# Performance work log

Measured on AMD Instinct MI355X. Metric: run time of the kernel, lower is better.

The kernel has to match this reference:

```python
import jax, jax.numpy as jnp
import numpy as np

TEMP = 0.1   # temperature
EPS = 1e-5   # BatchNorm eps
NEG = -1e9   # mask value for excluded logits

def _conv3x3(x, w):
    return jax.lax.conv_general_dilated(x, w, (1, 1), 'SAME',
                                        dimension_numbers=('NCHW', 'OIHW', 'NCHW'))

def _bn(x, gamma, beta, axes):
    # training-mode BatchNorm2d: stats over `axes` (per-sample (2,3) for the
    # single-sample anchor path, batch (0,2,3) for the dense-key path)
    m = x.mean(axes, keepdims=True)
    v = x.var(axes, keepdims=True)
    return gamma[None, :, None, None] * (x - m) * jax.lax.rsqrt(v + EPS) + beta[None, :, None, None]

def _encode(x, p, axes):
    # GranularityEncoder: conv3x3 -> BN -> ReLU -> conv1x1 -> BN -> ReLU -> GAP
    w1, g1, b1, w2, g2, b2 = p
    h = jax.nn.relu(_bn(_conv3x3(x, w1), g1, b1, axes))
    h = jnp.einsum('nchw,oc->nohw', h, w2)
    h = jax.nn.relu(_bn(h, g2, b2, axes))
    return h.mean((2, 3))  # [N, D]

def _norm(x):
    return x / jnp.maximum(jnp.linalg.norm(x, axis=-1, keepdims=True), 1e-12)

def _loss(sparse, dense, params, decision_mask):
    # Anchors: original encodes one sample at a time -> per-sample BN stats (2,3)
    Q = jnp.stack([_norm(_encode(s, p, (2, 3))) for s, p in zip(sparse, params)])        # [G,cav,D]
    # Dense keys: encoded as a full batch under no_grad -> batch BN stats, stop_gradient
    K = jax.lax.stop_gradient(
        jnp.stack([_norm(_encode(d, p, (0, 2, 3))) for d, p in zip(dense, params)]))     # [G,cav,D]
    S = jnp.einsum('gid,gjd->gij', Q, K)                     # same-granularity sims
    pos = jnp.diagonal(S, axis1=1, axis2=2)                  # [G,cav] l_pos
    cav = S.shape[1]
    S_m = jnp.where(jnp.eye(cav, dtype=bool)[None], NEG, S)  # inter-agent negatives (j != i)
    X = jnp.einsum('gid,hid->gih', Q, K)                     # cross-granularity, same agent
    X_m = jnp.where(jnp.eye(3, dtype=bool)[:, None, :], NEG, X)
    logits = jnp.concatenate([pos[..., None], S_m, X_m], axis=-1) / TEMP  # [G,cav,1+cav+3]
    loss_tab = -logits[..., 0] + jax.nn.logsumexp(logits, axis=-1)        # CE with label 0
    # The per-element loss only depends on (agent, granularity): weight by mask counts.
    cnt = jnp.stack([(decision_mask == g + 1).sum((1, 2)) for g in range(3)]).astype(jnp.float32)  # [G,cav-1]
    cnt = jnp.pad(cnt, ((0, 0), (1, 0)))  # agent 0 is never an anchor (loop starts at i=1)
    tot = cnt.sum()
    return jnp.where(tot > 0, (cnt * loss_tab).sum() / jnp.maximum(tot, 1.0), 0.0)

def setup_inputs():
    key = jax.random.key(0)
    ks = jax.random.split(key, 16)
    CAV, H, W, D = 5, 256, 256, 128
    C = {'g1': 64, 'g2': 32, 'g3': 16}
    inp = {}
    i = 0
    for name, c in C.items():
        inp['sparse_' + name] = jax.random.normal(ks[i], (CAV, c, H, W), jnp.float32); i += 1
        inp['dense_' + name] = jax.random.normal(ks[i], (CAV, c, H, W), jnp.float32); i += 1
        inp['w1_' + name] = jax.random.normal(ks[i], (64, c, 3, 3), jnp.float32) * 0.05; i += 1
        inp['bn1_gamma_' + name] = jnp.ones((64,), jnp.float32)
        inp['bn1_beta_' + name] = jnp.zeros((64,), jnp.float32)
        inp['w2_' + name] = jax.random.normal(ks[i], (D, 64), jnp.float32) * 0.05; i += 1
        inp['bn2_gamma_' + name] = jnp.ones((D,), jnp.float32)
        inp['bn2_beta_' + name] = jnp.zeros((D,), jnp.float32)
    inp['decision_mask'] = jax.random.randint(ks[i], (CAV - 1, 128, 128), 0, 4, jnp.int32)
    return inp

def reference(sparse_g1, dense_g1, w1_g1, bn1_gamma_g1, bn1_beta_g1, w2_g1, bn2_gamma_g1, bn2_beta_g1,
              sparse_g2, dense_g2, w1_g2, bn1_gamma_g2, bn1_beta_g2, w2_g2, bn2_gamma_g2, bn2_beta_g2,
              sparse_g3, dense_g3, w1_g3, bn1_gamma_g3, bn1_beta_g3, w2_g3, bn2_gamma_g3, bn2_beta_g3,
              decision_mask):
    sparse = [sparse_g1, sparse_g2, sparse_g3]
    dense = [dense_g1, dense_g2, dense_g3]
    params = [(w1_g1, bn1_gamma_g1, bn1_beta_g1, w2_g1, bn2_gamma_g1, bn2_beta_g1),
              (w1_g2, bn1_gamma_g2, bn1_beta_g2, w2_g2, bn2_gamma_g2, bn2_beta_g2),
              (w1_g3, bn1_gamma_g3, bn1_beta_g3, w2_g3, bn2_gamma_g3, bn2_beta_g3)]
    return _loss(sparse, dense, params, decision_mask)
```

## Files before the change

### kernel.cpp

```cpp
#include <hip/hip_runtime.h>
#include <math.h>

#define HW 65536
#define NS 5
#define DFEAT 128
#define CMID 64
#define TEMPER 0.1f
#define BNEPS 1e-5f

#define SWZ(a) ((a) ^ ((((a) >> 7) & 7) << 4))

typedef __attribute__((ext_vector_type(8))) short bf16x8;
typedef __attribute__((ext_vector_type(4))) float f32x4;

__device__ inline short f2bf(float f) {
  union { float f; unsigned u; } v; v.f = f;
  unsigned r = v.u + 0x7fffu + ((v.u >> 16) & 1u);
  return (short)(r >> 16);
}
__device__ inline float bf2f(unsigned short h) {
  union { unsigned u; float f; } v; v.u = ((unsigned)h) << 16;
  return v.f;
}

union U16B { int4 v; unsigned short s[8]; };

__global__ void zero_kernel(float* __restrict__ p, int n) {
  int i = blockIdx.x * blockDim.x + threadIdx.x;
  if (i < n) p[i] = 0.f;
}

template<int C, int CP>
__global__ __launch_bounds__(256) void transpose_kernel(const float* __restrict__ x,
                                                        unsigned short* __restrict__ xT,
                                                        float* __restrict__ st) {
  __shared__ float t[64 * (CP + 1)];
  const int tid = threadIdx.x;
  if (blockIdx.x == 0 && blockIdx.y == 0) {
    for (int i = tid; i < 1920; i += 256) st[i] = 0.f;
  }
  const int n = blockIdx.y;
  const int pix0 = blockIdx.x * 64;
  const float* xn = x + (size_t)n * C * HW + pix0;
#pragma unroll
  for (int it = 0; it < CP * 64 / 256; ++it) {
    int idx = it * 256 + tid;
    int c = idx >> 6, pix = idx & 63;
    float v = (c < C) ? xn[(size_t)c * HW + pix] : 0.f;
    t[pix * (CP + 1) + c] = v;
  }
  __syncthreads();
  unsigned* out = (unsigned*)(xT + ((size_t)n * HW + pix0) * CP);
#pragma unroll
  for (int it = 0; it < 64 * CP / 2 / 256; ++it) {
    int idx = it * 256 + tid;
    int cp = idx & (CP / 2 - 1), pix = idx / (CP / 2);
    float f0 = t[pix * (CP + 1) + 2 * cp];
    float f1 = t[pix * (CP + 1) + 2 * cp + 1];
    unsigned u = ((unsigned)(unsigned short)f2bf(f0)) |
                 (((unsigned)(unsigned short)f2bf(f1)) << 16);
    out[pix * (CP / 2) + cp] = u;
  }
}

template<int C, int CP>
__global__ void wprep_kernel(const float* __restrict__ w1, const float* __restrict__ w2,
                             unsigned short* __restrict__ w1p, unsigned short* __restrict__ w2p) {
  const int KS = CP / 32;
  const int total1 = 9 * KS * 2 * 64 * 32;
  int idx = blockIdx.x * 256 + threadIdx.x;
  if (idx < total1) {
    int kl = idx & 31; int tmp = idx >> 5;
    int nn = tmp & 63; tmp >>= 6;
    int hl = tmp & 1;  tmp >>= 1;
    int ks = tmp % KS; int s = tmp / KS;
    int ic = ks * 32 + kl;
    float v = (ic < C) ? w1[((size_t)nn * C + ic) * 9 + s] : 0.f;
    short hi = f2bf(v);
    short r = (hl == 0) ? hi : f2bf(v - bf2f((unsigned short)hi));
    w1p[idx] = (unsigned short)r;
  } else if (idx < total1 + 2 * 2 * 128 * 32) {
    int i2 = idx - total1;
    int kl = i2 & 31;
    int nn = (i2 >> 5) & 127;
    int hl = (i2 >> 12) & 1;
    int ks = i2 >> 13;
    float v = w2[nn * 64 + ks * 32 + kl];
    short hi = f2bf(v);
    short r = (hl == 0) ? hi : f2bf(v - bf2f((unsigned short)hi));
    w2p[i2] = (unsigned short)r;
  }
}

template<int CP>
__global__ __launch_bounds__(256, 2) void conv_mfma_kernel(
    const unsigned short* __restrict__ xT,
    const unsigned short* __restrict__ w1p,
    unsigned short* __restrict__ h1,
    float* __restrict__ st)
{
  const int KS = CP / 32;
  constexpr int XSB = 10 * 34 * CP * 2;
  constexpr int HSB = 256 * 64 * 2;
  constexpr int UNI = (XSB > HSB) ? XSB : HSB;
  __shared__ __align__(16) char smem[UNI];
  __shared__ float reds[4][64], redq[4][64];

  const int tid = threadIdx.x;
  const int lane = tid & 63, wave = tid >> 6;
  const int lanen = lane & 15, quad = lane >> 4;
  const int tx = blockIdx.x, ty = blockIdx.y, n = blockIdx.z;
  const int x0 = tx * 32, y0 = ty * 8;

  const int ROWB = 34 * CP * 2;
  const int xstart = (tx == 0) ? 1 : 0;
  const int xend = (tx == 7) ? 33 : 34;
  for (int r = wave; r < 10; r += 4) {
    int gy = y0 - 1 + r;
    const int rowbase = r * ROWB;
    if ((unsigned)gy >= 256u) {
      for (int ofs = lane * 16; ofs < ROWB; ofs += 1024) {
        int la = rowbase + ofs;
        *(int4*)(smem + SWZ(la)) = make_int4(0, 0, 0, 0);
      }
    } else {
      const char* g = (const char*)(xT + ((size_t)n * HW + gy * 256 + x0 - 1 + xstart) * CP);
      int nbytes = (xend - xstart) * CP * 2;
      int dst0 = rowbase + xstart * CP * 2;
      for (int ofs = lane * 16; ofs < nbytes; ofs += 1024) {
        int la = dst0 + ofs;
        *(int4*)(smem + SWZ(la)) = *(const int4*)(g + ofs);
      }
      if (xstart == 1) {
        for (int ofs = lane * 16; ofs < CP * 2; ofs += 1024) {
          int la = rowbase + ofs;
          *(int4*)(smem + SWZ(la)) = make_int4(0, 0, 0, 0);
        }
      }
      if (xend == 33) {
        for (int ofs = lane * 16; ofs < CP * 2; ofs += 1024) {
          int la = rowbase + 33 * CP * 2 + ofs;
          *(int4*)(smem + SWZ(la)) = make_int4(0, 0, 0, 0);
        }
      }
    }
  }
  __syncthreads();

  f32x4 acc[4][4];
#pragma unroll
  for (int t = 0; t < 4; ++t)
#pragma unroll
    for (int nt = 0; nt < 4; ++nt)
      acc[t][nt] = (f32x4){0.f, 0.f, 0.f, 0.f};

  int pbase[4];
#pragma unroll
  for (int t = 0; t < 4; ++t) {
    int p = wave * 64 + t * 16 + lanen;
    pbase[t] = (p >> 5) * 34 + (p & 31);
  }

#pragma unroll
  for (int s = 0; s < 9; ++s) {
    const int dy = s / 3, dx = s % 3;
#pragma unroll
    for (int ks = 0; ks < KS; ++ks) {
      bf16x8 af[4];
#pragma unroll
      for (int t = 0; t < 4; ++t) {
        int la = (pbase[t] + dy * 34 + dx) * (CP * 2) + ks * 64 + quad * 16;
        af[t] = *(const bf16x8*)(smem + SWZ(la));
      }
#pragma unroll
      for (int hl = 0; hl < 2; ++hl) {
        const unsigned short* wb = w1p + ((((s * KS + ks) * 2 + hl) * 64) + lanen) * 32 + quad * 8;
#pragma unroll
        for (int nt = 0; nt < 4; ++nt) {
          bf16x8 bf = *(const bf16x8*)(wb + nt * 16 * 32);
#pragma unroll
          for (int t = 0; t < 4; ++t)
            acc[t][nt] = __builtin_amdgcn_mfma_f32_16x16x32_bf16(af[t], bf, acc[t][nt], 0, 0, 0);
        }
      }
    }
  }

#pragma unroll
  for (int nt = 0; nt < 4; ++nt) {
    float s = 0.f, q = 0.f;
#pragma unroll
    for (int t = 0; t < 4; ++t)
#pragma unroll
      for (int r = 0; r < 4; ++r) {
        float v = acc[t][nt][r];
        s += v; q += v * v;
      }
    s += __shfl_xor(s, 16); s += __shfl_xor(s, 32);
    q += __shfl_xor(q, 16); q += __shfl_xor(q, 32);
    if (lane < 16) { reds[wave][nt * 16 + lanen] = s; redq[wave][nt * 16 + lanen] = q; }
  }
  __syncthreads();
  if (tid < 64) {
    float s = reds[0][tid] + reds[1][tid] + reds[2][tid] + reds[3][tid];
    float q = redq[0][tid] + redq[1][tid] + redq[2][tid] + redq[3][tid];
    atomicAdd(&st[(n * 64 + tid) * 2 + 0], s);
    atomicAdd(&st[(n * 64 + tid) * 2 + 1], q);
  }

#pragma unroll
  for (int t = 0; t < 4; ++t)
#pragma unroll
    for (int nt = 0; nt < 4; ++nt)
#pragma unroll
      for (int r = 0; r < 4; ++r) {
        int pix = wave * 64 + t * 16 + quad * 4 + r;
        int la = pix * 128 + (nt * 16 + lanen) * 2;
        *(unsigned short*)(smem + SWZ(la)) = (unsigned short)f2bf(acc[t][nt][r]);
      }
  __syncthreads();
#pragma unroll
  for (int it = 0; it < 8; ++it) {
    int idx = it * 256 + tid;
    int ocg = idx & 7, pix = idx >> 3;
    int py = pix >> 5, px = pix & 31;
    int la = pix * 128 + ocg * 16;
    int4 v = *(const int4*)(smem + SWZ(la));
    *(int4*)(h1 + ((size_t)n * HW + (y0 + py) * 256 + x0 + px) * 64 + ocg * 8) = v;
  }
}

__device__ inline void bn_pair(const float* __restrict__ st, const float* __restrict__ gamma,
                               const float* __restrict__ beta, int nch, int n, int ch,
                               int batchmode, float& a, float& b) {
  float s, q, cnt;
  if (batchmode) {
    s = 0.f; q = 0.f;
    for (int m = 0; m < NS; ++m) { s += st[(m * nch + ch) * 2]; q += st[(m * nch + ch) * 2 + 1]; }
    cnt = (float)NS * (float)HW;
  } else {
    s = st[(n * nch + ch) * 2]; q = st[(n * nch + ch) * 2 + 1];
    cnt = (float)HW;
  }
  float mean = s / cnt;
  float var = q / cnt - mean * mean;
  float inv = rsqrtf(var + BNEPS);
  a = gamma[ch] * inv;
  b = beta[ch] - mean * a;
}

template<bool GAP>
__global__ __launch_bounds__(256, 2) void stage2_mfma_kernel(
    const unsigned short* __restrict__ h1,
    const unsigned short* __restrict__ w2p,
    const float* __restrict__ st1, const float* __restrict__ gm1, const float* __restrict__ bt1,
    const float* __restrict__ st2, const float* __restrict__ gm2, const float* __restrict__ bt2,
    int batchmode,
    float* __restrict__ out)
{
  __shared__ __align__(16) char acts[256 * 64 * 2];
  __shared__ float red[4][128], redq[4][128];
  __shared__ float s_a1[64], s_b1[64], s_a2[128], s_b2[128];
  const int tid = threadIdx.x;
  const int lane = tid & 63, wave = tid >> 6;
  const int lanen = lane & 15, quad = lane >> 4;
  const int n = blockIdx.y;
  const int pix0 = blockIdx.x * 256;

  if (tid < 64) {
    float a, b;
    bn_pair(st1, gm1, bt1, CMID, n, tid, batchmode, a, b);
    s_a1[tid] = a; s_b1[tid] = b;
  }
  if constexpr (GAP) {
    if (tid >= 64 && tid < 192) {
      int ch = tid - 64;
      float a, b;
      bn_pair(st2, gm2, bt2, DFEAT, n, ch, batchmode, a, b);
      s_a2[ch] = a; s_b2[ch] = b;
    }
  }
  __syncthreads();

  const int cg = tid & 7;
  float a1c[8], b1c[8];
#pragma unroll
  for (int j = 0; j < 8; ++j) {
    a1c[j] = s_a1[cg * 8 + j];
    b1c[j] = s_b1[cg * 8 + j];
  }
  const unsigned short* hb = h1 + ((size_t)n * HW + pix0) * 64;
#pragma unroll
  for (int it = 0; it < 8; ++it) {
    int idx = it * 256 + tid;
    int pix = idx >> 3;
    U16B in, o;
    in.v = *(const int4*)(hb + pix * 64 + cg * 8);
#pragma unroll
    for (int j = 0; j < 8; ++j) {
      float f = bf2f(in.s[j]);
      o.s[j] = (unsigned short)f2bf(fmaxf(a1c[j] * f + b1c[j], 0.f));
    }
    int la = pix * 128 + cg * 16;
    *(int4*)(acts + SWZ(la)) = o.v;
  }
  __syncthreads();

  f32x4 acc[4][8];
#pragma unroll
  for (int mt = 0; mt < 4; ++mt)
#pragma unroll
    for (int nt = 0; nt < 8; ++nt)
      acc[mt][nt] = (f32x4){0.f, 0.f, 0.f, 0.f};

#pragma unroll
  for (int ks = 0; ks < 2; ++ks) {
    bf16x8 af[4];
#pragma unroll
    for (int mt = 0; mt < 4; ++mt) {
      int la = (wave * 64 + mt * 16 + lanen) * 128 + ks * 64 + quad * 16;
      af[mt] = *(const bf16x8*)(acts + SWZ(la));
    }
#pragma unroll
    for (int hl = 0; hl < 2; ++hl) {
      const unsigned short* wb = w2p + (((ks * 2 + hl) * 128) + lanen) * 32 + quad * 8;
#pragma unroll
      for (int nt = 0; nt < 8; ++nt) {
        bf16x8 bf = *(const bf16x8*)(wb + nt * 16 * 32);
#pragma unroll
        for (int mt = 0; mt < 4; ++mt)
          acc[mt][nt] = __builtin_amdgcn_mfma_f32_16x16x32_bf16(af[mt], bf, acc[mt][nt], 0, 0, 0);
      }
    }
  }

  if constexpr (GAP) {
#pragma unroll
    for (int nt = 0; nt < 8; ++nt) {
      int o = nt * 16 + lanen;
      float a2v = s_a2[o], b2v = s_b2[o];
      float s = 0.f;
#pragma unroll
      for (int mt = 0; mt < 4; ++mt)
#pragma unroll
        for (int r = 0; r < 4; ++r)
          s += fmaxf(a2v * acc[mt][nt][r] + b2v, 0.f);
      s += __shfl_xor(s, 16); s += __shfl_xor(s, 32);
      if (lane < 16) red[wave][o] = s;
    }
    __syncthreads();
    if (tid < 128)
      atomicAdd(&out[n * DFEAT + tid], red[0][tid] + red[1][tid] + red[2][tid] + red[3][tid]);
  } else {
#pragma unroll
    for (int nt = 0; nt < 8; ++nt) {
      int o = nt * 16 + lanen;
      float s = 0.f, q = 0.f;
#pragma unroll
      for (int mt = 0; mt < 4; ++mt)
#pragma unroll
        for (int r = 0; r < 4; ++r) {
          float v = acc[mt][nt][r];
          s += v; q += v * v;
        }
      s += __shfl_xor(s, 16); s += __shfl_xor(s, 32);
      q += __shfl_xor(q, 16); q += __shfl_xor(q, 32);
      if (lane < 16) { red[wave][o] = s; redq[wave][o] = q; }
    }
    __syncthreads();
    if (tid < 128) {
      atomicAdd(&out[(n * DFEAT + tid) * 2 + 0], red[0][tid] + red[1][tid] + red[2][tid] + red[3][tid]);
      atomicAdd(&out[(n * DFEAT + tid) * 2 + 1], redq[0][tid] + redq[1][tid] + redq[2][tid] + redq[3][tid]);
    }
  }
}

__global__ void feat_kernel(const float* __restrict__ gap, float* __restrict__ QK) {
  int b = blockIdx.x;
  int e = b / 5, n = b % 5;
  int g = e >> 1, br = e & 1;
  int d = threadIdx.x;
  float v = gap[(e * 5 + n) * DFEAT + d] * (1.0f / (float)HW);
  float q = v * v;
  for (int off = 32; off; off >>= 1) q += __shfl_down(q, off, 64);
  __shared__ float r2[2];
  if ((d & 63) == 0) r2[d >> 6] = q;
  __syncthreads();
  float nrm = sqrtf(r2[0] + r2[1]);
  float inv = 1.0f / fmaxf(nrm, 1e-12f);
  QK[((br * 3 + g) * 5 + n) * DFEAT + d] = v * inv;
}

__global__ __launch_bounds__(256) void loss_kernel(const float* __restrict__ QK,
                                                   const int* __restrict__ dm,
                                                   float* __restrict__ out)
{
  __shared__ float Qs[1920], Ks[1920];
  __shared__ float S[75], X[45], cnt[15], ltab[15];
  const int tid = threadIdx.x;
  for (int i = tid; i < 1920; i += 256) { Qs[i] = QK[i]; Ks[i] = QK[1920 + i]; }
  if (tid < 15) cnt[tid] = 0.f;
  __syncthreads();
  if (tid < 75) {
    int g = tid / 25, i = (tid / 5) % 5, j = tid % 5;
    const float* q = &Qs[(g * 5 + i) * 128];
    const float* k = &Ks[(g * 5 + j) * 128];
    float s = 0.f;
    for (int d = 0; d < 128; ++d) s += q[d] * k[d];
    S[tid] = s;
  } else if (tid < 120) {
    int u = tid - 75;
    int g = u / 15, i = (u % 15) / 3, h = u % 3;
    const float* q = &Qs[(g * 5 + i) * 128];
    const float* k = &Ks[(h * 5 + i) * 128];
    float s = 0.f;
    for (int d = 0; d < 128; ++d) s += q[d] * k[d];
    X[u] = s;
  }
  {
    int a = tid >> 6, l = tid & 63;
    int c0 = 0, c1 = 0, c2 = 0;
    const int* base = dm + a * 16384;
    for (int k = 0; k < 256; ++k) {
      int v = base[k * 64 + l];
      c0 += (v == 1); c1 += (v == 2); c2 += (v == 3);
    }
    atomicAdd(&cnt[0 * 5 + a + 1], (float)c0);
    atomicAdd(&cnt[1 * 5 + a + 1], (float)c1);
    atomicAdd(&cnt[2 * 5 + a + 1], (float)c2);
  }
  __syncthreads();
  if (tid < 15) {
    int g = tid / 5, i = tid % 5;
    const float inv_t = 1.0f / TEMPER;
    float lg[9];
    lg[0] = S[g * 25 + i * 5 + i] * inv_t;
    for (int j = 0; j < 5; ++j) lg[1 + j] = (j == i) ? (-1e9f * inv_t) : S[g * 25 + i * 5 + j] * inv_t;
    for (int h = 0; h < 3; ++h) lg[6 + h] = (h == g) ? (-1e9f * inv_t) : X[g * 15 + i * 3 + h] * inv_t;
    float m = lg[0];
    for (int k = 1; k < 9; ++k) m = fmaxf(m, lg[k]);
    float se = 0.f;
    for (int k = 0; k < 9; ++k) se += expf(lg[k] - m);
    ltab[tid] = -lg[0] + m + logf(se);
  }
  __syncthreads();
  if (tid == 0) {
    float tot = 0.f, acc = 0.f;
    for (int k = 0; k < 15; ++k) { tot += cnt[k]; acc += cnt[k] * ltab[k]; }
    out[0] = (tot > 0.f) ? acc / fmaxf(tot, 1.f) : 0.f;
  }
}

extern "C" void kernel_launch(void* const* d_in, const int* in_sizes, int n_in,
                              void* d_out, int out_size, void* d_ws, size_t ws_size,
                              hipStream_t stream) {
  (void)in_sizes; (void)n_in; (void)out_size; (void)ws_size;

  const float* sp[3]  = {(const float*)d_in[0],  (const float*)d_in[8],  (const float*)d_in[16]};
  const float* dn[3]  = {(const float*)d_in[1],  (const float*)d_in[9],  (const float*)d_in[17]};
  const float* w1[3]  = {(const float*)d_in[2],  (const float*)d_in[10], (const float*)d_in[18]};
  const float* gm1[3] = {(const float*)d_in[3],  (const float*)d_in[11], (const float*)d_in[19]};
  const float* bt1[3] = {(const float*)d_in[4],  (const float*)d_in[12], (const float*)d_in[20]};
  const float* w2[3]  = {(const float*)d_in[5],  (const float*)d_in[13], (const float*)d_in[21]};
  const float* gm2[3] = {(const float*)d_in[6],  (const float*)d_in[14], (const float*)d_in[22]};
  const float* bt2[3] = {(const float*)d_in[7],  (const float*)d_in[15], (const float*)d_in[23]};
  const int*   dm     = (const int*)d_in[24];

  float* ws_f = (float*)d_ws;
  unsigned short* h1u  = (unsigned short*)ws_f;
  unsigned short* xTu  = (unsigned short*)(ws_f + 10485760);
  unsigned short* w1pu = (unsigned short*)(ws_f + 20971520);
  unsigned short* w2pu = (unsigned short*)(ws_f + 20971520 + 36864);
  float* st1 = ws_f + 20971520 + 36864 + 8192;
  float* st2 = st1 + 640;
  float* gap = st2 + 1280;
  float* QK  = gap + 3840;

  zero_kernel<<<15, 256, 0, stream>>>(gap, 3840);

  for (int g = 0; g < 3; ++g) {
    if (g == 0)      wprep_kernel<64, 64><<<(9*2*2*64*32 + 16384 + 255)/256, 256, 0, stream>>>(w1[g], w2[g], w1pu, w2pu);
    else if (g == 1) wprep_kernel<32, 32><<<(9*1*2*64*32 + 16384 + 255)/256, 256, 0, stream>>>(w1[g], w2[g], w1pu, w2pu);
    else             wprep_kernel<16, 32><<<(9*1*2*64*32 + 16384 + 255)/256, 256, 0, stream>>>(w1[g], w2[g], w1pu, w2pu);

    for (int br = 0; br < 2; ++br) {
      const int e = g * 2 + br;
      const float* x = br ? dn[g] : sp[g];

      if (g == 0)      transpose_kernel<64, 64><<<dim3(1024, 5), 256, 0, stream>>>(x, xTu, st1);
      else if (g == 1) transpose_kernel<32, 32><<<dim3(1024, 5), 256, 0, stream>>>(x, xTu, st1);
      else             transpose_kernel<16, 32><<<dim3(1024, 5), 256, 0, stream>>>(x, xTu, st1);

      if (g == 0) conv_mfma_kernel<64><<<dim3(8, 32, 5), 256, 0, stream>>>(xTu, w1pu, h1u, st1);
      else        conv_mfma_kernel<32><<<dim3(8, 32, 5), 256, 0, stream>>>(xTu, w1pu, h1u, st1);

      stage2_mfma_kernel<false><<<dim3(256, 5), 256, 0, stream>>>(
          h1u, w2pu, st1, gm1[g], bt1[g], nullptr, nullptr, nullptr, br, st2);
      stage2_mfma_kernel<true><<<dim3(256, 5), 256, 0, stream>>>(
          h1u, w2pu, st1, gm1[g], bt1[g], st2, gm2[g], bt2[g], br, gap + e * 640);
    }
  }

  feat_kernel<<<30, 128, 0, stream>>>(gap, QK);
  loss_kernel<<<1, 256, 0, stream>>>(QK, dm, (float*)d_out);
}
```

Measured before the change: 1.284 ms.

## Double-buffer conv weights in registers and stage 1x1 weights in LDS

The 3x3 conv MFMA kernel now prefetches the next tap's weight fragments into a register double buffer while computing the current tap, which hides global load latency. The stage-2 kernel copies the split-bf16 1x1 weights (32KB) into swizzled shared memory once per block and reads B fragments from LDS instead of global memory. It reuses the activation buffer for the reduction scratch and adds a barrier to keep that safe. The register buffer raises VGPR pressure, which may limit occupancy or cause spills, and the extra 32KB of LDS per block may reduce the number of resident blocks.

```diff
diff --git a/kernel.cpp b/kernel.cpp
--- a/kernel.cpp
+++ b/kernel.cpp
@@ -99,7 +99,8 @@
     unsigned short* __restrict__ h1,
     float* __restrict__ st)
 {
-  const int KS = CP / 32;
+  constexpr int KS = CP / 32;
+  constexpr int NB = KS * 8;
   constexpr int XSB = 10 * 34 * CP * 2;
   constexpr int HSB = 256 * 64 * 2;
   constexpr int UNI = (XSB > HSB) ? XSB : HSB;
@@ -145,6 +146,16 @@
       }
     }
   }
+
+  const unsigned short* wlane = w1p + lanen * 32 + quad * 8;
+#define W1OFF(S, K, H, N) ((((((S) * KS + (K)) * 2 + (H)) * 64) + (N) * 16) * 32)
+  bf16x8 bw[2][NB];
+#pragma unroll
+  for (int i = 0; i < NB; ++i) {
+    int ks = i >> 3, hl = (i >> 2) & 1, nt = i & 3;
+    bw[0][i] = *(const bf16x8*)(wlane + W1OFF(0, ks, hl, nt));
+  }
+
   __syncthreads();
 
   f32x4 acc[4][4];
@@ -163,6 +174,14 @@
 
 #pragma unroll
   for (int s = 0; s < 9; ++s) {
+    const int cur = s & 1, nxt = cur ^ 1;
+    if (s < 8) {
+#pragma unroll
+      for (int i = 0; i < NB; ++i) {
+        int ks = i >> 3, hl = (i >> 2) & 1, nt = i & 3;
+        bw[nxt][i] = *(const bf16x8*)(wlane + W1OFF(s + 1, ks, hl, nt));
+      }
+    }
     const int dy = s / 3, dx = s % 3;
 #pragma unroll
     for (int ks = 0; ks < KS; ++ks) {
@@ -174,10 +193,9 @@
       }
 #pragma unroll
       for (int hl = 0; hl < 2; ++hl) {
-        const unsigned short* wb = w1p + ((((s * KS + ks) * 2 + hl) * 64) + lanen) * 32 + quad * 8;
 #pragma unroll
         for (int nt = 0; nt < 4; ++nt) {
-          bf16x8 bf = *(const bf16x8*)(wb + nt * 16 * 32);
+          bf16x8 bf = bw[cur][ks * 8 + hl * 4 + nt];
 #pragma unroll
           for (int t = 0; t < 4; ++t)
             acc[t][nt] = __builtin_amdgcn_mfma_f32_16x16x32_bf16(af[t], bf, acc[t][nt], 0, 0, 0);
@@ -185,6 +203,7 @@
       }
     }
   }
+#undef W1OFF
 
 #pragma unroll
   for (int nt = 0; nt < 4; ++nt) {
@@ -258,14 +277,25 @@
     int batchmode,
     float* __restrict__ out)
 {
-  __shared__ __align__(16) char acts[256 * 64 * 2];
-  __shared__ float red[4][128], redq[4][128];
+  __shared__ __align__(16) char acts[256 * 128];
+  __shared__ __align__(16) char w2s[32768];
   __shared__ float s_a1[64], s_b1[64], s_a2[128], s_b2[128];
+  float* red  = (float*)acts;
+  float* redq = red + 512;
   const int tid = threadIdx.x;
   const int lane = tid & 63, wave = tid >> 6;
   const int lanen = lane & 15, quad = lane >> 4;
   const int n = blockIdx.y;
   const int pix0 = blockIdx.x * 256;
+
+  {
+    const char* src = (const char*)w2p;
+#pragma unroll
+    for (int j = 0; j < 8; ++j) {
+      int la = (tid * 8 + j) * 16;
+      *(int4*)(w2s + SWZ(la)) = *(const int4*)(src + la);
+    }
+  }
 
   if (tid < 64) {
     float a, b;
@@ -323,16 +353,17 @@
     }
 #pragma unroll
     for (int hl = 0; hl < 2; ++hl) {
-      const unsigned short* wb = w2p + (((ks * 2 + hl) * 128) + lanen) * 32 + quad * 8;
 #pragma unroll
       for (int nt = 0; nt < 8; ++nt) {
-        bf16x8 bf = *(const bf16x8*)(wb + nt * 16 * 32);
+        int lb = (((ks * 2 + hl) * 128) + nt * 16 + lanen) * 64 + quad * 16;
+        bf16x8 bf = *(const bf16x8*)(w2s + SWZ(lb));
 #pragma unroll
         for (int mt = 0; mt < 4; ++mt)
           acc[mt][nt] = __builtin_amdgcn_mfma_f32_16x16x32_bf16(af[mt], bf, acc[mt][nt], 0, 0, 0);
       }
     }
   }
+  __syncthreads();
 
   if constexpr (GAP) {
 #pragma unroll
@@ -346,11 +377,12 @@
         for (int r = 0; r < 4; ++r)
           s += fmaxf(a2v * acc[mt][nt][r] + b2v, 0.f);
       s += __shfl_xor(s, 16); s += __shfl_xor(s, 32);
-      if (lane < 16) red[wave][o] = s;
+      if (lane < 16) red[wave * 128 + o] = s;
     }
     __syncthreads();
     if (tid < 128)
-      atomicAdd(&out[n * DFEAT + tid], red[0][tid] + red[1][tid] + red[2][tid] + red[3][tid]);
+      atomicAdd(&out[n * DFEAT + tid],
+                red[tid] + red[128 + tid] + red[256 + tid] + red[384 + tid]);
   } else {
 #pragma unroll
     for (int nt = 0; nt < 8; ++nt) {
@@ -365,12 +397,14 @@
         }
       s += __shfl_xor(s, 16); s += __shfl_xor(s, 32);
       q += __shfl_xor(q, 16); q += __shfl_xor(q, 32);
-      if (lane < 16) { red[wave][o] = s; redq[wave][o] = q; }
+      if (lane < 16) { red[wave * 128 + o] = s; redq[wave * 128 + o] = q; }
     }
     __syncthreads();
     if (tid < 128) {
-      atomicAdd(&out[(n * DFEAT + tid) * 2 + 0], red[0][tid] + red[1][tid] + red[2][tid] + red[3][tid]);
-      atomicAdd(&out[(n * DFEAT + tid) * 2 + 1], redq[0][tid] + redq[1][tid] + redq[2][tid] + redq[3][tid]);
+      atomicAdd(&out[(n * DFEAT + tid) * 2 + 0],
+                red[tid] + red[128 + tid] + red[256 + tid] + red[384 + tid]);
+      atomicAdd(&out[(n * DFEAT + tid) * 2 + 1],
+                redq[tid] + redq[128 + tid] + redq[256 + tid] + redq[384 + tid]);
     }
   }
 }
```

Result: faster. 1.224 ms (-4.7%).

## Drop LDS staging in conv and stage2, use zero-padded input and direct global loads

Applied to the files above, without the earlier changes.

The transposed input is written into a zero-bordered 258x258 padded layout, so the 3x3 conv kernel can read A fragments straight from global/L2 with no halo staging in LDS and no bounds checks. The conv output is packed and stored directly from registers, with the MFMA operand order swapped to suit this. Stage2 applies BN1+ReLU in registers on the directly loaded tile and drops its LDS buffer. Tiles are halved and occupancy hints raised. The cost is repeated 9x global reads of overlapping input, which relies on cache hits instead of LDS reuse.

```diff
diff --git a/kernel.cpp b/kernel.cpp
--- a/kernel.cpp
+++ b/kernel.cpp
@@ -7,8 +7,8 @@
 #define CMID 64
 #define TEMPER 0.1f
 #define BNEPS 1e-5f
-
-#define SWZ(a) ((a) ^ ((((a) >> 7) & 7) << 4))
+#define PW 258
+#define PPITCH (258*258)
 
 typedef __attribute__((ext_vector_type(8))) short bf16x8;
 typedef __attribute__((ext_vector_type(4))) float f32x4;
@@ -22,12 +22,31 @@
   union { unsigned u; float f; } v; v.u = ((unsigned)h) << 16;
   return v.f;
 }
-
-union U16B { int4 v; unsigned short s[8]; };
+__device__ inline unsigned pack2bf(float a, float b) {
+  return ((unsigned)(unsigned short)f2bf(a)) | (((unsigned)(unsigned short)f2bf(b)) << 16);
+}
+
+union U16B { int4 v; unsigned short s[8]; bf16x8 b; };
 
 __global__ void zero_kernel(float* __restrict__ p, int n) {
   int i = blockIdx.x * blockDim.x + threadIdx.x;
   if (i < n) p[i] = 0.f;
+}
+
+template<int CP>
+__global__ void border_zero_kernel(unsigned short* __restrict__ xT) {
+  const int PPX = CP / 8;
+  int idx = blockIdx.x * 256 + threadIdx.x;
+  if (idx >= 5 * 1028 * PPX) return;
+  int c = idx % PPX;
+  int p = idx / PPX;
+  int n = p / 1028, b = p % 1028;
+  int row, col;
+  if (b < 258)      { row = 0;       col = b; }
+  else if (b < 516) { row = 257;     col = b - 258; }
+  else if (b < 772) { row = b - 515; col = 0; }
+  else              { row = b - 771; col = 257; }
+  *(int4*)(xT + ((size_t)n * PPITCH + row * PW + col) * CP + c * 8) = make_int4(0, 0, 0, 0);
 }
 
 template<int C, int CP>
@@ -50,7 +69,8 @@
     t[pix * (CP + 1) + c] = v;
   }
   __syncthreads();
-  unsigned* out = (unsigned*)(xT + ((size_t)n * HW + pix0) * CP);
+  const int gy = pix0 >> 8, gx0 = pix0 & 255;
+  unsigned* out = (unsigned*)(xT + ((size_t)n * PPITCH + (size_t)(gy + 1) * PW + gx0 + 1) * CP);
 #pragma unroll
   for (int it = 0; it < 64 * CP / 2 / 256; ++it) {
     int idx = it * 256 + tid;
@@ -93,17 +113,13 @@
 }
 
 template<int CP>
-__global__ __launch_bounds__(256, 2) void conv_mfma_kernel(
-    const unsigned short* __restrict__ xT,
+__global__ __launch_bounds__(256, 4) void conv_mfma_kernel(
+    const unsigned short* __restrict__ xTp,
     const unsigned short* __restrict__ w1p,
     unsigned short* __restrict__ h1,
     float* __restrict__ st)
 {
-  const int KS = CP / 32;
-  constexpr int XSB = 10 * 34 * CP * 2;
-  constexpr int HSB = 256 * 64 * 2;
-  constexpr int UNI = (XSB > HSB) ? XSB : HSB;
-  __shared__ __align__(16) char smem[UNI];
+  constexpr int KS = CP / 32;
   __shared__ float reds[4][64], redq[4][64];
 
   const int tid = threadIdx.x;
@@ -112,93 +128,60 @@
   const int tx = blockIdx.x, ty = blockIdx.y, n = blockIdx.z;
   const int x0 = tx * 32, y0 = ty * 8;
 
-  const int ROWB = 34 * CP * 2;
-  const int xstart = (tx == 0) ? 1 : 0;
-  const int xend = (tx == 7) ? 33 : 34;
-  for (int r = wave; r < 10; r += 4) {
-    int gy = y0 - 1 + r;
-    const int rowbase = r * ROWB;
-    if ((unsigned)gy >= 256u) {
-      for (int ofs = lane * 16; ofs < ROWB; ofs += 1024) {
-        int la = rowbase + ofs;
-        *(int4*)(smem + SWZ(la)) = make_int4(0, 0, 0, 0);
-      }
-    } else {
-      const char* g = (const char*)(xT + ((size_t)n * HW + gy * 256 + x0 - 1 + xstart) * CP);
-      int nbytes = (xend - xstart) * CP * 2;
-      int dst0 = rowbase + xstart * CP * 2;
-      for (int ofs = lane * 16; ofs < nbytes; ofs += 1024) {
-        int la = dst0 + ofs;
-        *(int4*)(smem + SWZ(la)) = *(const int4*)(g + ofs);
-      }
-      if (xstart == 1) {
-        for (int ofs = lane * 16; ofs < CP * 2; ofs += 1024) {
-          int la = rowbase + ofs;
-          *(int4*)(smem + SWZ(la)) = make_int4(0, 0, 0, 0);
+  const unsigned short* xb = xTp + (size_t)n * PPITCH * CP;
+
+  int pbase[4];
+#pragma unroll
+  for (int t = 0; t < 4; ++t) {
+    int prow = y0 + wave * 2 + (t >> 1);
+    int pcol = x0 + (t & 1) * 16 + lanen;
+    pbase[t] = prow * PW + pcol;
+  }
+
+  f32x4 acc[4][4];
+#pragma unroll
+  for (int t = 0; t < 4; ++t)
+#pragma unroll
+    for (int nt = 0; nt < 4; ++nt)
+      acc[t][nt] = (f32x4){0.f, 0.f, 0.f, 0.f};
+
+#pragma unroll
+  for (int s = 0; s < 9; ++s) {
+    const int dy = s / 3, dx = s % 3;
+#pragma unroll
+    for (int ks = 0; ks < KS; ++ks) {
+      bf16x8 af[4];
+#pragma unroll
+      for (int t = 0; t < 4; ++t)
+        af[t] = *(const bf16x8*)(xb + (size_t)(pbase[t] + dy * PW + dx) * CP + ks * 32 + quad * 8);
+      const unsigned short* wb = w1p + (((s * KS + ks) * 2) * 64 + lanen) * 32 + quad * 8;
+#pragma unroll
+      for (int hl = 0; hl < 2; ++hl) {
+#pragma unroll
+        for (int nt = 0; nt < 4; ++nt) {
+          bf16x8 bf = *(const bf16x8*)(wb + (hl * 64 + nt * 16) * 32);
+#pragma unroll
+          for (int t = 0; t < 4; ++t)
+            acc[t][nt] = __builtin_amdgcn_mfma_f32_16x16x32_bf16(bf, af[t], acc[t][nt], 0, 0, 0);
         }
       }
-      if (xend == 33) {
-        for (int ofs = lane * 16; ofs < CP * 2; ofs += 1024) {
-          int la = rowbase + 33 * CP * 2 + ofs;
-          *(int4*)(smem + SWZ(la)) = make_int4(0, 0, 0, 0);
-        }
+    }
+  }
+
+#pragma unroll
+  for (int nt = 0; nt < 4; ++nt) {
+#pragma unroll
+    for (int r = 0; r < 4; ++r) {
+      float v0 = acc[0][nt][r], v1 = acc[1][nt][r], v2 = acc[2][nt][r], v3 = acc[3][nt][r];
+      float sv = v0 + v1 + v2 + v3;
+      float qv = v0 * v0 + v1 * v1 + v2 * v2 + v3 * v3;
+      sv += __shfl_xor(sv, 1); sv += __shfl_xor(sv, 2); sv += __shfl_xor(sv, 4); sv += __shfl_xor(sv, 8);
+      qv += __shfl_xor(qv, 1); qv += __shfl_xor(qv, 2); qv += __shfl_xor(qv, 4); qv += __shfl_xor(qv, 8);
+      if (lanen == 0) {
+        reds[wave][nt * 16 + quad * 4 + r] = sv;
+        redq[wave][nt * 16 + quad * 4 + r] = qv;
       }
     }
-  }
-  __syncthreads();
-
-  f32x4 acc[4][4];
-#pragma unroll
-  for (int t = 0; t < 4; ++t)
-#pragma unroll
-    for (int nt = 0; nt < 4; ++nt)
-      acc[t][nt] = (f32x4){0.f, 0.f, 0.f, 0.f};
-
-  int pbase[4];
-#pragma unroll
-  for (int t = 0; t < 4; ++t) {
-    int p = wave * 64 + t * 16 + lanen;
-    pbase[t] = (p >> 5) * 34 + (p & 31);
-  }
-
-#pragma unroll
-  for (int s = 0; s < 9; ++s) {
-    const int dy = s / 3, dx = s % 3;
-#pragma unroll
-    for (int ks = 0; ks < KS; ++ks) {
-      bf16x8 af[4];
-#pragma unroll
-      for (int t = 0; t < 4; ++t) {
-        int la = (pbase[t] + dy * 34 + dx) * (CP * 2) + ks * 64 + quad * 16;
-        af[t] = *(const bf16x8*)(smem + SWZ(la));
-      }
-#pragma unroll
-      for (int hl = 0; hl < 2; ++hl) {
-        const unsigned short* wb = w1p + ((((s * KS + ks) * 2 + hl) * 64) + lanen) * 32 + quad * 8;
-#pragma unroll
-        for (int nt = 0; nt < 4; ++nt) {
-          bf16x8 bf = *(const bf16x8*)(wb + nt * 16 * 32);
-#pragma unroll
-          for (int t = 0; t < 4; ++t)
-            acc[t][nt] = __builtin_amdgcn_mfma_f32_16x16x32_bf16(af[t], bf, acc[t][nt], 0, 0, 0);
-        }
-      }
-    }
-  }
-
-#pragma unroll
-  for (int nt = 0; nt < 4; ++nt) {
-    float s = 0.f, q = 0.f;
-#pragma unroll
-    for (int t = 0; t < 4; ++t)
-#pragma unroll
-      for (int r = 0; r < 4; ++r) {
-        float v = acc[t][nt][r];
-        s += v; q += v * v;
-      }
-    s += __shfl_xor(s, 16); s += __shfl_xor(s, 32);
-    q += __shfl_xor(q, 16); q += __shfl_xor(q, 32);
-    if (lane < 16) { reds[wave][nt * 16 + lanen] = s; redq[wave][nt * 16 + lanen] = q; }
   }
   __syncthreads();
   if (tid < 64) {
@@ -209,24 +192,16 @@
   }
 
 #pragma unroll
-  for (int t = 0; t < 4; ++t)
-#pragma unroll
-    for (int nt = 0; nt < 4; ++nt)
-#pragma unroll
-      for (int r = 0; r < 4; ++r) {
-        int pix = wave * 64 + t * 16 + quad * 4 + r;
-        int la = pix * 128 + (nt * 16 + lanen) * 2;
-        *(unsigned short*)(smem + SWZ(la)) = (unsigned short)f2bf(acc[t][nt][r]);
-      }
-  __syncthreads();
-#pragma unroll
-  for (int it = 0; it < 8; ++it) {
-    int idx = it * 256 + tid;
-    int ocg = idx & 7, pix = idx >> 3;
-    int py = pix >> 5, px = pix & 31;
-    int la = pix * 128 + ocg * 16;
-    int4 v = *(const int4*)(smem + SWZ(la));
-    *(int4*)(h1 + ((size_t)n * HW + (y0 + py) * 256 + x0 + px) * 64 + ocg * 8) = v;
+  for (int t = 0; t < 4; ++t) {
+    int pixf = (y0 + wave * 2 + (t >> 1)) * 256 + x0 + (t & 1) * 16 + lanen;
+    unsigned short* hp = h1 + ((size_t)n * HW + pixf) * 64 + quad * 4;
+#pragma unroll
+    for (int nt = 0; nt < 4; ++nt) {
+      uint2 u;
+      u.x = pack2bf(acc[t][nt][0], acc[t][nt][1]);
+      u.y = pack2bf(acc[t][nt][2], acc[t][nt][3]);
+      *(uint2*)(hp + nt * 16) = u;
+    }
   }
 }
 
@@ -250,7 +225,7 @@
 }
 
 template<bool GAP>
-__global__ __launch_bounds__(256, 2) void stage2_mfma_kernel(
+__global__ __launch_bounds__(256, 3) void stage2_mfma_kernel(
     const unsigned short* __restrict__ h1,
     const unsigned short* __restrict__ w2p,
     const float* __restrict__ st1, const float* __restrict__ gm1, const float* __restrict__ bt1,
@@ -258,14 +233,13 @@
     int batchmode,
     float* __restrict__ out)
 {
-  __shared__ __align__(16) char acts[256 * 64 * 2];
   __shared__ float red[4][128], redq[4][128];
   __shared__ float s_a1[64], s_b1[64], s_a2[128], s_b2[128];
   const int tid = threadIdx.x;
   const int lane = tid & 63, wave = tid >> 6;
   const int lanen = lane & 15, quad = lane >> 4;
   const int n = blockIdx.y;
-  const int pix0 = blockIdx.x * 256;
+  const int pix0 = blockIdx.x * 128;
 
   if (tid < 64) {
     float a, b;
@@ -282,44 +256,34 @@
   }
   __syncthreads();
 
-  const int cg = tid & 7;
-  float a1c[8], b1c[8];
-#pragma unroll
-  for (int j = 0; j < 8; ++j) {
-    a1c[j] = s_a1[cg * 8 + j];
-    b1c[j] = s_b1[cg * 8 + j];
-  }
-  const unsigned short* hb = h1 + ((size_t)n * HW + pix0) * 64;
-#pragma unroll
-  for (int it = 0; it < 8; ++it) {
-    int idx = it * 256 + tid;
-    int pix = idx >> 3;
-    U16B in, o;
-    in.v = *(const int4*)(hb + pix * 64 + cg * 8);
-#pragma unroll
-    for (int j = 0; j < 8; ++j) {
-      float f = bf2f(in.s[j]);
-      o.s[j] = (unsigned short)f2bf(fmaxf(a1c[j] * f + b1c[j], 0.f));
-    }
-    int la = pix * 128 + cg * 16;
-    *(int4*)(acts + SWZ(la)) = o.v;
-  }
-  __syncthreads();
-
-  f32x4 acc[4][8];
-#pragma unroll
-  for (int mt = 0; mt < 4; ++mt)
+  f32x4 acc[2][8];
+#pragma unroll
+  for (int mt = 0; mt < 2; ++mt)
 #pragma unroll
     for (int nt = 0; nt < 8; ++nt)
       acc[mt][nt] = (f32x4){0.f, 0.f, 0.f, 0.f};
 
+  const unsigned short* hb = h1 + ((size_t)n * HW + pix0) * 64;
+
 #pragma unroll
   for (int ks = 0; ks < 2; ++ks) {
-    bf16x8 af[4];
-#pragma unroll
-    for (int mt = 0; mt < 4; ++mt) {
-      int la = (wave * 64 + mt * 16 + lanen) * 128 + ks * 64 + quad * 16;
-      af[mt] = *(const bf16x8*)(acts + SWZ(la));
+    float a1c[8], b1c[8];
+#pragma unroll
+    for (int j = 0; j < 8; ++j) {
+      a1c[j] = s_a1[ks * 32 + quad * 8 + j];
+      b1c[j] = s_b1[ks * 32 + quad * 8 + j];
+    }
+    bf16x8 af[2];
+#pragma unroll
+    for (int mt = 0; mt < 2; ++mt) {
+      U16B in, o;
+      in.v = *(const int4*)(hb + (size_t)(wave * 32 + mt * 16 + lanen) * 64 + ks * 32 + quad * 8);
+#pragma unroll
+      for (int j = 0; j < 8; ++j) {
+        float f = bf2f(in.s[j]);
+        o.s[j] = (unsigned short)f2bf(fmaxf(a1c[j] * f + b1c[j], 0.f));
+      }
+      af[mt] = o.b;
     }
 #pragma unroll
     for (int hl = 0; hl < 2; ++hl) {
@@ -328,7 +292,7 @@
       for (int nt = 0; nt < 8; ++nt) {
         bf16x8 bf = *(const bf16x8*)(wb + nt * 16 * 32);
 #pragma unroll
-        for (int mt = 0; mt < 4; ++mt)
+        for (int mt = 0; mt < 2; ++mt)
           acc[mt][nt] = __builtin_amdgcn_mfma_f32_16x16x32_bf16(af[mt], bf, acc[mt][nt], 0, 0, 0);
       }
     }
@@ -341,7 +305,7 @@
       float a2v = s_a2[o], b2v = s_b2[o];
       float s = 0.f;
 #pragma unroll
-      for (int mt = 0; mt < 4; ++mt)
+      for (int mt = 0; mt < 2; ++mt)
 #pragma unroll
         for (int r = 0; r < 4; ++r)
           s += fmaxf(a2v * acc[mt][nt][r] + b2v, 0.f);
@@ -357,7 +321,7 @@
       int o = nt * 16 + lanen;
       float s = 0.f, q = 0.f;
 #pragma unroll
-      for (int mt = 0; mt < 4; ++mt)
+      for (int mt = 0; mt < 2; ++mt)
 #pragma unroll
         for (int r = 0; r < 4; ++r) {
           float v = acc[mt][nt][r];
@@ -469,9 +433,9 @@
   float* ws_f = (float*)d_ws;
   unsigned short* h1u  = (unsigned short*)ws_f;
   unsigned short* xTu  = (unsigned short*)(ws_f + 10485760);
-  unsigned short* w1pu = (unsigned short*)(ws_f + 20971520);
-  unsigned short* w2pu = (unsigned short*)(ws_f + 20971520 + 36864);
-  float* st1 = ws_f + 20971520 + 36864 + 8192;
+  unsigned short* w1pu = (unsigned short*)(ws_f + 21136000);
+  unsigned short* w2pu = (unsigned short*)(ws_f + 21136000 + 36864);
+  float* st1 = ws_f + 21136000 + 36864 + 8192;
   float* st2 = st1 + 640;
   float* gap = st2 + 1280;
   float* QK  = gap + 3840;
@@ -483,6 +447,9 @@
     else if (g == 1) wprep_kernel<32, 32><<<(9*1*2*64*32 + 16384 + 255)/256, 256, 0, stream>>>(w1[g], w2[g], w1pu, w2pu);
     else             wprep_kernel<16, 32><<<(9*1*2*64*32 + 16384 + 255)/256, 256, 0, stream>>>(w1[g], w2[g], w1pu, w2pu);
 
+    if (g == 0)      border_zero_kernel<64><<<(5*1028*8 + 255)/256, 256, 0, stream>>>(xTu);
+    else if (g == 1) border_zero_kernel<32><<<(5*1028*4 + 255)/256, 256, 0, stream>>>(xTu);
+
     for (int br = 0; br < 2; ++br) {
       const int e = g * 2 + br;
       const float* x = br ? dn[g] : sp[g];
@@ -494,9 +461,9 @@
       if (g == 0) conv_mfma_kernel<64><<<dim3(8, 32, 5), 256, 0, stream>>>(xTu, w1pu, h1u, st1);
       else        conv_mfma_kernel<32><<<dim3(8, 32, 5), 256, 0, stream>>>(xTu, w1pu, h1u, st1);
 
-      stage2_mfma_kernel<false><<<dim3(256, 5), 256, 0, stream>>>(
+      stage2_mfma_kernel<false><<<dim3(512, 5), 256, 0, stream>>>(
           h1u, w2pu, st1, gm1[g], bt1[g], nullptr, nullptr, nullptr, br, st2);
-      stage2_mfma_kernel<true><<<dim3(256, 5), 256, 0, stream>>>(
+      stage2_mfma_kernel<true><<<dim3(512, 5), 256, 0, stream>>>(
           h1u, w2pu, st1, gm1[g], bt1[g], st2, gm2[g], bt2[g], br, gap + e * 640);
     }
   }
```

Result: slower. 1.745 ms (+35.9%).
